# Kernel optimization log

Hardware: AMD Instinct MI355X
Metric: run time of the kernel (lower is better)

The kernel has to match this reference:

```python
import jax, jax.numpy as jnp
import numpy as np

T, B, IN_DIM, H, NB = 100, 1024, 40, 512, 4
WB, IB, ABMVM, ABNM = 8, 8, 8, 8


def _pact(x, a):
    # PACT clip sign(x)*min(|x|, a); a: (NB,) broadcast over (NB, B, D)
    a = a[:, None, None]
    return jnp.sign(x) * 0.5 * (jnp.abs(x) - jnp.abs(jnp.abs(x) - a) + a)


def _quant(x, bits, rng):
    step = 2.0 ** (bits - 1)
    x01 = jnp.clip(x / rng, -1.0 + 1.0 / step, 1.0 - 1.0 / step)
    return jnp.round(x01 * step) / step * rng


def _q(x, bits, a):
    # straight-through quantizer with per-block range a: (NB,)
    return x + jax.lax.stop_gradient(_quant(x, bits, a[:, None, None]) - x)


@jax.custom_vjp
def custom_mm(x, w, b):
    wc = jnp.clip(w, -1.0, 1.0)
    return jnp.einsum('nbi,nio->nbo', x, _quant(wc, WB, 1.0)) + _quant(b, WB, 1.0)


def _mm_fwd(x, w, b):
    wc = jnp.clip(w, -1.0, 1.0)
    out = jnp.einsum('nbi,nio->nbo', x, _quant(wc, WB, 1.0)) + _quant(b, WB, 1.0)
    return out, (x, wc)


def _mm_bwd(res, g):
    x, wc = res
    return (jnp.einsum('nbo,nio->nbi', g, wc),
            jnp.einsum('nbi,nbo->nio', x, g),
            g.sum(axis=1, keepdims=True))


custom_mm.defvjp(_mm_fwd, _mm_bwd)


def _forward(inputs, weight_ih, weight_hh, bias_ih, bias_hh, a_cell, fc_w, fc_b, fc_a):
    (a1, a2, a3, a4, a5, a6, a7, a8, a9,
     a10, a11, a12, a13, a14) = a_cell
    nb, hd = weight_hh.shape[0], weight_hh.shape[1]
    bsz = inputs.shape[1]

    def step(carry, x_t):
        hx, cx = carry
        xr = jnp.broadcast_to(x_t[None], (nb,) + x_t.shape)  # input.repeat(n_blocks,1,1)
        p1 = custom_mm(_q(_pact(xr, a1), IB, a1), weight_ih, bias_ih)
        p2 = custom_mm(_q(_pact(hx, a11), IB, a11), weight_hh, bias_hh)  # w_mask == ones (drop_p=0)
        pre = _q(_pact(p1, a12), ABMVM, a12) + _q(_pact(p2, a13), ABMVM, a13)
        gates = _q(_pact(pre, a14), ABNM, a14)  # (nb, B, 4H)
        i, j, f, o = jnp.split(gates, 4, axis=2)
        fg = _q(_pact(jax.nn.sigmoid(f), a3), ABNM, a3)
        ig = _q(_pact(jax.nn.sigmoid(i), a4), ABNM, a4)
        jg = _q(_pact(jnp.tanh(j), a5), ABNM, a5)
        og = _q(_pact(jax.nn.sigmoid(o), a6), ABNM, a6)
        gc = _q(_pact(cx * fg, a7), ABNM, a7)
        ai = _q(_pact(ig * jg, a8), ABNM, a8)
        nc = _q(_pact(gc + ai, a9), ABNM, a9)
        ac = _q(_pact(jnp.tanh(nc), a10), ABNM, a10)
        nh = _q(_pact(ac * og, a11), ABNM, a11)
        return (nh, nc), None

    h0 = jnp.zeros((nb, bsz, hd), inputs.dtype)
    (hT, _), _ = jax.lax.scan(step, (h0, h0), inputs)
    fa1, fa2 = fc_a
    fc = _q(_pact(custom_mm(_q(_pact(hT, fa1), IB, fa1), fc_w, fc_b), fa2), ABMVM, fa2)  # (nb, B, 3)
    return fc[:4].transpose(1, 0, 2).reshape(bsz, 12)


def setup_inputs():
    key = jax.random.key(0)
    k = jax.random.split(key, 4)
    lim_ih = 1.0 / np.sqrt(IN_DIM)
    lim_hh = 1.0 / np.sqrt(H)
    lim_fc = np.sqrt(6.0 / H)
    a_vals = jnp.array([128., 16., 1., 1., 1., 1., 4., 1., 4., 1., 4., 4., 4., 4.], jnp.float32)
    return {
        "inputs": jax.random.normal(k[0], (T, B, IN_DIM), jnp.float32),
        "weight_ih": jax.random.uniform(k[1], (NB, IN_DIM, 4 * H), jnp.float32, -lim_ih, lim_ih),
        "weight_hh": jax.random.uniform(k[2], (NB, H, 4 * H), jnp.float32, -lim_hh, lim_hh),
        "bias_ih": jnp.zeros((NB, 1, 4 * H), jnp.float32),
        "bias_hh": jnp.ones((NB, 1, 4 * H), jnp.float32),
        "a_cell": jnp.broadcast_to(a_vals[:, None], (14, NB)),
        "fc_w": jax.random.uniform(k[3], (NB, H, 3), jnp.float32, -lim_fc, lim_fc),
        "fc_b": jnp.zeros((NB, 1, 3), jnp.float32),
        "fc_a": jnp.broadcast_to(jnp.array([4., 16.], jnp.float32)[:, None], (2, NB)),
    }


def reference(inputs, weight_ih, weight_hh, bias_ih, bias_hh, a_cell, fc_w, fc_b, fc_a):
    return _forward(inputs, weight_ih, weight_hh, bias_ih, bias_hh, a_cell, fc_w, fc_b, fc_a)
```

## Files before the change

### kernel.cpp

```cpp
#include <hip/hip_runtime.h>
#include <math.h>

#define T_STEPS 100
#define BATCH   1024
#define INDIM   40
#define HID     512
#define NBLK    4
#define KPAD    576
#define NG      2048
#define LDAP    80

typedef int v4i __attribute__((ext_vector_type(4)));

__device__ __forceinline__ float pact_f(float x, float a){
    float u = fabsf(x);
    float v = fabsf(u - a);
    float s = (x > 0.f) ? 1.f : ((x < 0.f) ? -1.f : 0.f);
    return (s * 0.5f) * ((u - v) + a);
}
__device__ __forceinline__ int quant_int(float x, float inv_a){
    float xs = x * inv_a;
    xs = fminf(fmaxf(xs, -127.f/128.f), 127.f/128.f);
    return (int)rintf(xs * 128.f);
}
__device__ __forceinline__ int clamp127(int v){
    return v > 127 ? 127 : (v < -127 ? -127 : v);
}

#define SETUP_N0 (T_STEPS*BATCH*64)
#define SETUP_N1 (NBLK*NG*KPAD)
#define SETUP_N2 (NBLK*NG)
#define SETUP_N3 (NBLK*3*512)
#define SETUP_TOTAL (SETUP_N0 + SETUP_N1 + SETUP_N2 + SETUP_N3 + NBLK*3 + 255)

__global__ __launch_bounds__(256) void k_setup(const float* __restrict__ x,
                                               const float* __restrict__ wih,
                                               const float* __restrict__ whh,
                                               const float* __restrict__ bih,
                                               const float* __restrict__ bhh,
                                               const float* __restrict__ fcw,
                                               const float* __restrict__ fcb,
                                               signed char* __restrict__ xq,
                                               signed char* __restrict__ wt,
                                               int* __restrict__ bihq,
                                               int* __restrict__ bhhq,
                                               signed char* __restrict__ fcwt,
                                               int* __restrict__ fcbq,
                                               signed char* __restrict__ sigl,
                                               signed char* __restrict__ thl){
    for (long idx = blockIdx.x * 256 + threadIdx.x; idx < SETUP_TOTAL; idx += (long)gridDim.x * 256){
        long r = idx;
        if (r < SETUP_N0){
            int k = (int)(r & 63); long tb = r >> 6;
            signed char q = 0;
            if (k < INDIM){
                float xv = x[tb * INDIM + k];
                q = (signed char)quant_int(pact_f(xv, 128.f), 1.f/128.f);
            }
            xq[r] = q;
            continue;
        }
        r -= SETUP_N0;
        if (r < SETUP_N1){
            int kk = (int)(r % KPAD);
            int no = (int)(r / KPAD);
            int c  = no % NG;
            int n  = no / NG;
            int gate = (c >> 4) & 3;
            int h    = ((c >> 6) << 4) | (c & 15);
            int o    = gate * 512 + h;
            float w;
            if (kk < INDIM)      w = wih[((long)n*INDIM + kk)*NG + o];
            else if (kk < 64)    { wt[r] = 0; continue; }
            else                 w = whh[((long)n*HID + (kk-64))*NG + o];
            w = fminf(fmaxf(w, -1.f), 1.f);
            wt[r] = (signed char)quant_int(w, 1.f);
            continue;
        }
        r -= SETUP_N1;
        if (r < SETUP_N2){
            int c = (int)(r % NG); int n = (int)(r / NG);
            int gate = (c >> 4) & 3;
            int h    = ((c >> 6) << 4) | (c & 15);
            int o    = gate * 512 + h;
            bihq[r] = quant_int(bih[n*NG + o], 1.f);
            bhhq[r] = quant_int(bhh[n*NG + o], 1.f);
            continue;
        }
        r -= SETUP_N2;
        if (r < SETUP_N3){
            int k = (int)(r % 512); int nc = (int)(r / 512); int c = nc % 3; int n = nc / 3;
            float w = fcw[((long)n*HID + k)*3 + c];
            w = fminf(fmaxf(w, -1.f), 1.f);
            fcwt[r] = (signed char)quant_int(w, 1.f);
            continue;
        }
        r -= SETUP_N3;
        if (r < NBLK*3){
            fcbq[r] = quant_int(fcb[r], 1.f);
            continue;
        }
        r -= NBLK*3;
        {
            double xv = (double)((int)r - 127) / 32.0;
            float s = (float)(1.0 / (1.0 + exp(-xv)));
            float t = (float)tanh(xv);
            sigl[r] = (signed char)quant_int(pact_f(s, 1.f), 1.f);
            thl[r]  = (signed char)quant_int(pact_f(t, 1.f), 1.f);
        }
    }
}

__global__ __launch_bounds__(256, 2) void k_step(const signed char* __restrict__ xq_t,
                                                 const signed char* __restrict__ Hin,
                                                 signed char* __restrict__ Hout,
                                                 signed char* __restrict__ C,
                                                 const signed char* __restrict__ Wt,
                                                 const int* __restrict__ bihq,
                                                 const int* __restrict__ bhhq,
                                                 const signed char* __restrict__ sigl,
                                                 const signed char* __restrict__ thl){
    __shared__ __align__(16) signed char As[2][128*LDAP];
    __shared__ __align__(16) signed char Ws[2][128*LDAP];
    __shared__ signed char s_sig[256], s_th[256];

    int bid = blockIdx.x;
    int xcd = bid & 7, slot = bid >> 3;
    int n   = xcd >> 1;
    int idx = ((xcd & 1) << 6) | slot;
    int bm  = idx & 7;
    int bn  = idx >> 3;

    int tid  = threadIdx.x;
    int lane = tid & 63;
    int wave = tid >> 6;
    int wm = wave >> 1, wn = wave & 1;

    if (tid < 255){ s_sig[tid] = sigl[tid]; s_th[tid] = thl[tid]; }

    int hglob = bn*32 + wn*16 + (lane & 15);
    int rbase = bm*128 + wm*64 + ((lane >> 4) << 2);
    int cbase = bn*128 + wn*64 + (lane & 15);
    int b1v[4], b2v[4];
    #pragma unroll
    for (int ni = 0; ni < 4; ++ni){
        b1v[ni] = bihq[n*NG + cbase + ni*16];
        b2v[ni] = 32 * bhhq[n*NG + cbase + ni*16];
    }
    int* Cw = (int*)(C + ((long)(n*HID + hglob))*BATCH + rbase);
    int cold[4];
    #pragma unroll
    for (int mi = 0; mi < 4; ++mi) cold[mi] = Cw[mi*4];

    int  srow = tid >> 1;
    int  scol = (tid & 1) * 32;
    int  aoff = srow*LDAP + scol;
    const signed char* hrow = Hin + ((long)(n*BATCH + bm*128 + srow))*HID + scol;
    const signed char* wrow = Wt  + ((long)n*NG + bn*128 + srow)*KPAD + scol;

    int am = wm*64 + (lane & 15);
    int bo = wn*64 + (lane & 15);
    int ak = (lane >> 4) * 16;

    const signed char* xrow = xq_t + (bm*128 + srow)*64 + scol;
    int4 ra0 = *(const int4*)xrow;
    int4 ra1 = *(const int4*)(xrow + 16);
    int4 rw0 = *(const int4*)wrow;
    int4 rw1 = *(const int4*)(wrow + 16);

    v4i acc1[4][4] = {};
    v4i acc2[4][4] = {};
    int q12p[4][4];

    for (int kt = 0; kt < 9; ++kt){
        signed char* Ab = As[kt & 1];
        signed char* Wb = Ws[kt & 1];
        *(int4*)&Ab[aoff] = ra0; *(int4*)&Ab[aoff + 16] = ra1;
        *(int4*)&Wb[aoff] = rw0; *(int4*)&Wb[aoff + 16] = rw1;
        __syncthreads();
        if (kt < 8){
            ra0 = *(const int4*)(hrow + kt*64);
            ra1 = *(const int4*)(hrow + kt*64 + 16);
            rw0 = *(const int4*)(wrow + (kt+1)*64);
            rw1 = *(const int4*)(wrow + (kt+1)*64 + 16);
        }
        v4i af[4], bf[4];
        #pragma unroll
        for (int mi = 0; mi < 4; ++mi) af[mi] = *(const v4i*)&Ab[(am + mi*16)*LDAP + ak];
        #pragma unroll
        for (int ni = 0; ni < 4; ++ni) bf[ni] = *(const v4i*)&Wb[(bo + ni*16)*LDAP + ak];
        if (kt == 0){
            #pragma unroll
            for (int mi = 0; mi < 4; ++mi)
                #pragma unroll
                for (int ni = 0; ni < 4; ++ni)
                    acc1[mi][ni] = __builtin_amdgcn_mfma_i32_16x16x64_i8(af[mi], bf[ni], acc1[mi][ni], 0, 0, 0);
            #pragma unroll
            for (int mi = 0; mi < 4; ++mi)
                #pragma unroll
                for (int ni = 0; ni < 4; ++ni){
                    int pk = 0;
                    #pragma unroll
                    for (int r = 0; r < 4; ++r){
                        int q = clamp127((int)rintf((float)(acc1[mi][ni][r] + b1v[ni]) * 0.25f));
                        pk |= (q & 255) << (8*r);
                    }
                    q12p[mi][ni] = pk;
                }
        } else {
            #pragma unroll
            for (int mi = 0; mi < 4; ++mi)
                #pragma unroll
                for (int ni = 0; ni < 4; ++ni)
                    acc2[mi][ni] = __builtin_amdgcn_mfma_i32_16x16x64_i8(af[mi], bf[ni], acc2[mi][ni], 0, 0, 0);
        }
    }

    #pragma unroll
    for (int mi = 0; mi < 4; ++mi){
        int cw = cold[mi];
        int cnew = 0;
        #pragma unroll
        for (int r = 0; r < 4; ++r){
            int g4[4];
            #pragma unroll
            for (int ni = 0; ni < 4; ++ni){
                int S2  = acc2[mi][ni][r] + b2v[ni];
                int q13 = clamp127((int)rintf((float)S2 * 0.0078125f));
                int q12 = (signed char)(q12p[mi][ni] >> (8*r));
                g4[ni]  = clamp127(q12 + q13);
            }
            int ig = s_sig[g4[0] + 127];
            int jg = s_th [g4[1] + 127];
            int fg = s_sig[g4[2] + 127];
            int og = s_sig[g4[3] + 127];
            int cc = (signed char)(cw >> (8*r));
            int gc = clamp127((int)rintf((float)(cc * fg) * 0.0078125f));
            int ai = clamp127((int)rintf((float)(ig * jg) * 0.0078125f));
            int nc = clamp127((int)rintf((float)(4*gc + ai) * 0.25f));
            int ac = s_th[nc + 127];
            int nh = clamp127((int)rintf((float)(ac * og) * (1.0f/512.0f)));
            cnew |= (nc & 255) << (8*r);
            Hout[((long)(n*BATCH) + rbase + mi*16 + r)*HID + hglob] = (signed char)nh;
        }
        Cw[mi*4] = cnew;
    }
}

__global__ __launch_bounds__(256) void k_fc(const signed char* __restrict__ H,
                                            const signed char* __restrict__ fcwt,
                                            const int* __restrict__ fcbq,
                                            float* __restrict__ out){
    int wave = threadIdx.x >> 6, lane = threadIdx.x & 63;
    int nb = blockIdx.x * 4 + wave;
    int n = nb >> 10, b = nb & 1023;
    const signed char* h = H + (long)nb * HID + lane * 8;
    int2 hv = *(const int2*)h;
    int acc[3] = {0, 0, 0};
    #pragma unroll
    for (int c = 0; c < 3; ++c){
        const signed char* wp = fcwt + ((long)(n*3 + c))*512 + lane*8;
        int2 wv = *(const int2*)wp;
        int s = 0;
        #pragma unroll
        for (int e = 0; e < 4; ++e){
            s += (int)(signed char)(hv.x >> (8*e)) * (int)(signed char)(wv.x >> (8*e));
            s += (int)(signed char)(hv.y >> (8*e)) * (int)(signed char)(wv.y >> (8*e));
        }
        acc[c] = s;
    }
    #pragma unroll
    for (int off = 32; off; off >>= 1){
        acc[0] += __shfl_down(acc[0], off, 64);
        acc[1] += __shfl_down(acc[1], off, 64);
        acc[2] += __shfl_down(acc[2], off, 64);
    }
    if (lane == 0){
        #pragma unroll
        for (int c = 0; c < 3; ++c){
            int v = acc[c] + 32 * fcbq[n*3 + c];
            int q = clamp127((int)rintf((float)v * (1.0f/512.0f)));
            out[b*12 + n*3 + c] = (float)q * 0.125f;
        }
    }
}

extern "C" void kernel_launch(void* const* d_in, const int* in_sizes, int n_in,
                              void* d_out, int out_size, void* d_ws, size_t ws_size,
                              hipStream_t stream)
{
    const float* x   = (const float*)d_in[0];
    const float* wih = (const float*)d_in[1];
    const float* whh = (const float*)d_in[2];
    const float* bih = (const float*)d_in[3];
    const float* bhh = (const float*)d_in[4];
    const float* fcw = (const float*)d_in[6];
    const float* fcb = (const float*)d_in[7];
    float* out = (float*)d_out;
    (void)in_sizes; (void)n_in; (void)out_size; (void)ws_size;

    char* p = (char*)d_ws;
    auto alloc = [&](size_t nbytes){ char* r = p; p += (nbytes + 255) & ~(size_t)255; return r; };
    signed char* Xq   = (signed char*)alloc((size_t)T_STEPS*BATCH*64);
    signed char* Wt   = (signed char*)alloc((size_t)NBLK*NG*KPAD);
    signed char* Hb0  = (signed char*)alloc((size_t)NBLK*BATCH*HID);
    signed char* Hb1  = (signed char*)alloc((size_t)NBLK*BATCH*HID);
    signed char* Cb   = (signed char*)alloc((size_t)NBLK*BATCH*HID);
    int*         bihq = (int*)alloc((size_t)NBLK*NG*4);
    int*         bhhq = (int*)alloc((size_t)NBLK*NG*4);
    signed char* fcwt = (signed char*)alloc((size_t)NBLK*3*512);
    int*         fcbq = (int*)alloc((size_t)NBLK*3*4);
    signed char* sigl = (signed char*)alloc(256);
    signed char* thl  = (signed char*)alloc(256);

    k_setup<<<2048, 256, 0, stream>>>(x, wih, whh, bih, bhh, fcw, fcb,
                                      Xq, Wt, bihq, bhhq, fcwt, fcbq, sigl, thl);
    hipMemsetAsync(Hb0, 0, (size_t)3*NBLK*BATCH*HID, stream);

    for (int t = 0; t < T_STEPS; ++t){
        const signed char* Hi = (t & 1) ? Hb1 : Hb0;
        signed char*       Ho = (t & 1) ? Hb0 : Hb1;
        k_step<<<512, 256, 0, stream>>>(Xq + (size_t)t*BATCH*64, Hi, Ho, Cb, Wt, bihq, bhhq, sigl, thl);
    }
    k_fc<<<(NBLK*BATCH)/4, 256, 0, stream>>>(Hb0, fcwt, fcbq, out);
}
```

Before: 1.261 ms.

## Fuse timestep launches into one persistent kernel with group barriers

Replaces the 100 per-timestep kernel launches with a single persistent kernel that loops over time. Blocks sharing a (block-matrix, batch-tile) row group synchronise through a global atomic counter with release/acquire fences. The cell state stays in registers across steps instead of round-tripping through global memory. This relies on all 512 blocks being co-resident (two per CU at the launch bound) and adds spin-wait barrier latency each step.

```diff
diff --git a/kernel.cpp b/kernel.cpp
--- a/kernel.cpp
+++ b/kernel.cpp
@@ -111,15 +111,15 @@
     }
 }
 
-__global__ __launch_bounds__(256, 2) void k_step(const signed char* __restrict__ xq_t,
-                                                 const signed char* __restrict__ Hin,
-                                                 signed char* __restrict__ Hout,
-                                                 signed char* __restrict__ C,
-                                                 const signed char* __restrict__ Wt,
-                                                 const int* __restrict__ bihq,
-                                                 const int* __restrict__ bhhq,
-                                                 const signed char* __restrict__ sigl,
-                                                 const signed char* __restrict__ thl){
+__global__ __launch_bounds__(256, 2) void k_persist(const signed char* __restrict__ Xq,
+                                                    signed char* __restrict__ H0,
+                                                    signed char* __restrict__ H1,
+                                                    const signed char* __restrict__ Wt,
+                                                    const int* __restrict__ bihq,
+                                                    const int* __restrict__ bhhq,
+                                                    const signed char* __restrict__ sigl,
+                                                    const signed char* __restrict__ thl,
+                                                    unsigned* __restrict__ bar){
     __shared__ __align__(16) signed char As[2][128*LDAP];
     __shared__ __align__(16) signed char Ws[2][128*LDAP];
     __shared__ signed char s_sig[256], s_th[256];
@@ -147,103 +147,123 @@
         b1v[ni] = bihq[n*NG + cbase + ni*16];
         b2v[ni] = 32 * bhhq[n*NG + cbase + ni*16];
     }
-    int* Cw = (int*)(C + ((long)(n*HID + hglob))*BATCH + rbase);
-    int cold[4];
-    #pragma unroll
-    for (int mi = 0; mi < 4; ++mi) cold[mi] = Cw[mi*4];
+    int cold[4] = {0,0,0,0};
 
     int  srow = tid >> 1;
     int  scol = (tid & 1) * 32;
     int  aoff = srow*LDAP + scol;
-    const signed char* hrow = Hin + ((long)(n*BATCH + bm*128 + srow))*HID + scol;
-    const signed char* wrow = Wt  + ((long)n*NG + bn*128 + srow)*KPAD + scol;
+    const signed char* hrow0 = H0 + ((long)(n*BATCH + bm*128 + srow))*HID + scol;
+    const signed char* hrow1 = H1 + ((long)(n*BATCH + bm*128 + srow))*HID + scol;
+    const signed char* wrow  = Wt + ((long)n*NG + bn*128 + srow)*KPAD + scol;
+    const signed char* xbase = Xq + (bm*128 + srow)*64 + scol;
+    signed char* hob0 = H1 + (long)(n*BATCH)*HID;
+    signed char* hob1 = H0 + (long)(n*BATCH)*HID;
 
     int am = wm*64 + (lane & 15);
     int bo = wn*64 + (lane & 15);
     int ak = (lane >> 4) * 16;
-
-    const signed char* xrow = xq_t + (bm*128 + srow)*64 + scol;
-    int4 ra0 = *(const int4*)xrow;
-    int4 ra1 = *(const int4*)(xrow + 16);
-    int4 rw0 = *(const int4*)wrow;
-    int4 rw1 = *(const int4*)(wrow + 16);
-
-    v4i acc1[4][4] = {};
-    v4i acc2[4][4] = {};
-    int q12p[4][4];
-
-    for (int kt = 0; kt < 9; ++kt){
-        signed char* Ab = As[kt & 1];
-        signed char* Wb = Ws[kt & 1];
-        *(int4*)&Ab[aoff] = ra0; *(int4*)&Ab[aoff + 16] = ra1;
-        *(int4*)&Wb[aoff] = rw0; *(int4*)&Wb[aoff + 16] = rw1;
-        __syncthreads();
-        if (kt < 8){
-            ra0 = *(const int4*)(hrow + kt*64);
-            ra1 = *(const int4*)(hrow + kt*64 + 16);
-            rw0 = *(const int4*)(wrow + (kt+1)*64);
-            rw1 = *(const int4*)(wrow + (kt+1)*64 + 16);
-        }
-        v4i af[4], bf[4];
+    int g  = ((n << 3) | bm) * 32;
+
+    for (int t = 0; t < T_STEPS; ++t){
+        const signed char* hrow  = (t & 1) ? hrow1 : hrow0;
+        signed char*       houtb = (t & 1) ? hob1 : hob0;
+
+        const signed char* xr = xbase + (long)t * (BATCH*64);
+        int4 ra0 = *(const int4*)xr;
+        int4 ra1 = *(const int4*)(xr + 16);
+        int4 rw0 = *(const int4*)wrow;
+        int4 rw1 = *(const int4*)(wrow + 16);
+
+        if (t){
+            __syncthreads();
+            if (tid == 0){
+                __builtin_amdgcn_fence(__ATOMIC_RELEASE, "agent");
+                atomicAdd(&bar[g], 1u);
+                unsigned tgt = 16u * (unsigned)t;
+                while (__hip_atomic_load(&bar[g], __ATOMIC_RELAXED, __HIP_MEMORY_SCOPE_AGENT) < tgt)
+                    __builtin_amdgcn_s_sleep(1);
+                __builtin_amdgcn_fence(__ATOMIC_ACQUIRE, "agent");
+            }
+            __syncthreads();
+        }
+
+        v4i acc1[4][4] = {};
+        v4i acc2[4][4] = {};
+        int q12p[4][4];
+
+        for (int kt = 0; kt < 9; ++kt){
+            signed char* Ab = As[kt & 1];
+            signed char* Wb = Ws[kt & 1];
+            *(int4*)&Ab[aoff] = ra0; *(int4*)&Ab[aoff + 16] = ra1;
+            *(int4*)&Wb[aoff] = rw0; *(int4*)&Wb[aoff + 16] = rw1;
+            __syncthreads();
+            if (kt < 8){
+                ra0 = *(const int4*)(hrow + kt*64);
+                ra1 = *(const int4*)(hrow + kt*64 + 16);
+                rw0 = *(const int4*)(wrow + (kt+1)*64);
+                rw1 = *(const int4*)(wrow + (kt+1)*64 + 16);
+            }
+            v4i af[4], bf[4];
+            #pragma unroll
+            for (int mi = 0; mi < 4; ++mi) af[mi] = *(const v4i*)&Ab[(am + mi*16)*LDAP + ak];
+            #pragma unroll
+            for (int ni = 0; ni < 4; ++ni) bf[ni] = *(const v4i*)&Wb[(bo + ni*16)*LDAP + ak];
+            if (kt == 0){
+                #pragma unroll
+                for (int mi = 0; mi < 4; ++mi)
+                    #pragma unroll
+                    for (int ni = 0; ni < 4; ++ni)
+                        acc1[mi][ni] = __builtin_amdgcn_mfma_i32_16x16x64_i8(af[mi], bf[ni], acc1[mi][ni], 0, 0, 0);
+                #pragma unroll
+                for (int mi = 0; mi < 4; ++mi)
+                    #pragma unroll
+                    for (int ni = 0; ni < 4; ++ni){
+                        int pk = 0;
+                        #pragma unroll
+                        for (int r = 0; r < 4; ++r){
+                            int q = clamp127((int)rintf((float)(acc1[mi][ni][r] + b1v[ni]) * 0.25f));
+                            pk |= (q & 255) << (8*r);
+                        }
+                        q12p[mi][ni] = pk;
+                    }
+            } else {
+                #pragma unroll
+                for (int mi = 0; mi < 4; ++mi)
+                    #pragma unroll
+                    for (int ni = 0; ni < 4; ++ni)
+                        acc2[mi][ni] = __builtin_amdgcn_mfma_i32_16x16x64_i8(af[mi], bf[ni], acc2[mi][ni], 0, 0, 0);
+            }
+        }
+
         #pragma unroll
-        for (int mi = 0; mi < 4; ++mi) af[mi] = *(const v4i*)&Ab[(am + mi*16)*LDAP + ak];
-        #pragma unroll
-        for (int ni = 0; ni < 4; ++ni) bf[ni] = *(const v4i*)&Wb[(bo + ni*16)*LDAP + ak];
-        if (kt == 0){
+        for (int mi = 0; mi < 4; ++mi){
+            int cw = cold[mi];
+            int cnew = 0;
             #pragma unroll
-            for (int mi = 0; mi < 4; ++mi)
-                #pragma unroll
-                for (int ni = 0; ni < 4; ++ni)
-                    acc1[mi][ni] = __builtin_amdgcn_mfma_i32_16x16x64_i8(af[mi], bf[ni], acc1[mi][ni], 0, 0, 0);
-            #pragma unroll
-            for (int mi = 0; mi < 4; ++mi)
+            for (int r = 0; r < 4; ++r){
+                int g4[4];
                 #pragma unroll
                 for (int ni = 0; ni < 4; ++ni){
-                    int pk = 0;
-                    #pragma unroll
-                    for (int r = 0; r < 4; ++r){
-                        int q = clamp127((int)rintf((float)(acc1[mi][ni][r] + b1v[ni]) * 0.25f));
-                        pk |= (q & 255) << (8*r);
-                    }
-                    q12p[mi][ni] = pk;
+                    int S2  = acc2[mi][ni][r] + b2v[ni];
+                    int q13 = clamp127((int)rintf((float)S2 * 0.0078125f));
+                    int q12 = (signed char)(q12p[mi][ni] >> (8*r));
+                    g4[ni]  = clamp127(q12 + q13);
                 }
-        } else {
-            #pragma unroll
-            for (int mi = 0; mi < 4; ++mi)
-                #pragma unroll
-                for (int ni = 0; ni < 4; ++ni)
-                    acc2[mi][ni] = __builtin_amdgcn_mfma_i32_16x16x64_i8(af[mi], bf[ni], acc2[mi][ni], 0, 0, 0);
-        }
-    }
-
-    #pragma unroll
-    for (int mi = 0; mi < 4; ++mi){
-        int cw = cold[mi];
-        int cnew = 0;
-        #pragma unroll
-        for (int r = 0; r < 4; ++r){
-            int g4[4];
-            #pragma unroll
-            for (int ni = 0; ni < 4; ++ni){
-                int S2  = acc2[mi][ni][r] + b2v[ni];
-                int q13 = clamp127((int)rintf((float)S2 * 0.0078125f));
-                int q12 = (signed char)(q12p[mi][ni] >> (8*r));
-                g4[ni]  = clamp127(q12 + q13);
-            }
-            int ig = s_sig[g4[0] + 127];
-            int jg = s_th [g4[1] + 127];
-            int fg = s_sig[g4[2] + 127];
-            int og = s_sig[g4[3] + 127];
-            int cc = (signed char)(cw >> (8*r));
-            int gc = clamp127((int)rintf((float)(cc * fg) * 0.0078125f));
-            int ai = clamp127((int)rintf((float)(ig * jg) * 0.0078125f));
-            int nc = clamp127((int)rintf((float)(4*gc + ai) * 0.25f));
-            int ac = s_th[nc + 127];
-            int nh = clamp127((int)rintf((float)(ac * og) * (1.0f/512.0f)));
-            cnew |= (nc & 255) << (8*r);
-            Hout[((long)(n*BATCH) + rbase + mi*16 + r)*HID + hglob] = (signed char)nh;
-        }
-        Cw[mi*4] = cnew;
+                int ig = s_sig[g4[0] + 127];
+                int jg = s_th [g4[1] + 127];
+                int fg = s_sig[g4[2] + 127];
+                int og = s_sig[g4[3] + 127];
+                int cc = (signed char)(cw >> (8*r));
+                int gc = clamp127((int)rintf((float)(cc * fg) * 0.0078125f));
+                int ai = clamp127((int)rintf((float)(ig * jg) * 0.0078125f));
+                int nc = clamp127((int)rintf((float)(4*gc + ai) * 0.25f));
+                int ac = s_th[nc + 127];
+                int nh = clamp127((int)rintf((float)(ac * og) * (1.0f/512.0f)));
+                cnew |= (nc & 255) << (8*r);
+                houtb[(long)(rbase + mi*16 + r)*HID + hglob] = (signed char)nh;
+            }
+            cold[mi] = cnew;
+        }
     }
 }
 
@@ -305,22 +325,19 @@
     signed char* Wt   = (signed char*)alloc((size_t)NBLK*NG*KPAD);
     signed char* Hb0  = (signed char*)alloc((size_t)NBLK*BATCH*HID);
     signed char* Hb1  = (signed char*)alloc((size_t)NBLK*BATCH*HID);
-    signed char* Cb   = (signed char*)alloc((size_t)NBLK*BATCH*HID);
     int*         bihq = (int*)alloc((size_t)NBLK*NG*4);
     int*         bhhq = (int*)alloc((size_t)NBLK*NG*4);
     signed char* fcwt = (signed char*)alloc((size_t)NBLK*3*512);
     int*         fcbq = (int*)alloc((size_t)NBLK*3*4);
     signed char* sigl = (signed char*)alloc(256);
     signed char* thl  = (signed char*)alloc(256);
+    unsigned*    bar  = (unsigned*)alloc(32*32*4);
 
     k_setup<<<2048, 256, 0, stream>>>(x, wih, whh, bih, bhh, fcw, fcb,
                                       Xq, Wt, bihq, bhhq, fcwt, fcbq, sigl, thl);
-    hipMemsetAsync(Hb0, 0, (size_t)3*NBLK*BATCH*HID, stream);
-
-    for (int t = 0; t < T_STEPS; ++t){
-        const signed char* Hi = (t & 1) ? Hb1 : Hb0;
-        signed char*       Ho = (t & 1) ? Hb0 : Hb1;
-        k_step<<<512, 256, 0, stream>>>(Xq + (size_t)t*BATCH*64, Hi, Ho, Cb, Wt, bihq, bhhq, sigl, thl);
-    }
+    hipMemsetAsync(Hb0, 0, (size_t)2*NBLK*BATCH*HID, stream);
+    hipMemsetAsync(bar, 0, 32*32*4, stream);
+
+    k_persist<<<512, 256, 0, stream>>>(Xq, Hb0, Hb1, Wt, bihq, bhhq, sigl, thl, bar);
     k_fc<<<(NBLK*BATCH)/4, 256, 0, stream>>>(Hb0, fcwt, fcbq, out);
 }
```

Measured after the change: 2.831 ms. +124.6%, slower.
